# Kernel optimization log

Hardware: AMD Instinct MI355X
Metric: run time of the kernel (lower is better)

Reference implementation:

```python
import jax, jax.numpy as jnp
import numpy as np

N = 65536
E = 1048576
IN_DIM, HID, OUT = 500, 256, 64
ALPHA = 0.1
K = 10


def setup_inputs() -> dict:
    key = jax.random.key(0)
    ks = jax.random.split(key, 12)
    x = jax.random.normal(ks[0], (N, IN_DIM), dtype=jnp.float32)
    edge_row = jax.random.randint(ks[1], (E,), 0, N, dtype=jnp.int32)
    edge_col = jax.random.randint(ks[2], (E,), 0, N, dtype=jnp.int32)
    edge_weight = jax.random.uniform(ks[3], (E,), dtype=jnp.float32)
    # Linear params (Kaiming-uniform-like scale)
    def lin(k, fan_in, fan_out):
        kw, kb = jax.random.split(k)
        bound = 1.0 / np.sqrt(fan_in)
        W = jax.random.uniform(kw, (fan_in, fan_out), minval=-bound, maxval=bound, dtype=jnp.float32)
        b = jax.random.uniform(kb, (fan_out,), minval=-bound, maxval=bound, dtype=jnp.float32)
        return W, b
    W1, b1 = lin(ks[4], IN_DIM, HID)
    W2, b2 = lin(ks[5], HID, HID)
    W3, b3 = lin(ks[6], HID, OUT)
    return {"x": x, "W1": W1, "b1": b1, "W2": W2, "b2": b2,
            "W3": W3, "b3": b3, "edge_weight": edge_weight,
            "edge_row": edge_row, "edge_col": edge_col}


def reference(x, W1, b1, W2, b2, W3, b3, edge_weight, edge_row, edge_col):
    # MLP stack (dropout=0.0, norm_type='none')
    h = jax.nn.relu(x @ W1 + b1)          # [N, HID]
    h = jax.nn.relu(h @ W2 + b2)          # [N, HID]
    h = h @ W3 + b3                        # [N, OUT]
    h0 = h
    w = edge_weight[:, None]               # [E, 1]
    # APPNP: k steps of h = (1-alpha) * (A @ h) + alpha * h0 (SpMM via segment_sum)
    def step(h, _):
        msg = h[edge_col] * w               # [E, OUT] gather + scale
        agg = jax.ops.segment_sum(msg, edge_row, num_segments=N)  # [N, OUT]
        return (1.0 - ALPHA) * agg + ALPHA * h0, None
    h, _ = jax.lax.scan(step, h, None, length=K)
    return h
```

## Files before the change

### kernel.cpp

```cpp
#include <hip/hip_runtime.h>
#include <cstdint>
#include <cstddef>


#define N_NODES   65536
#define N_EDGES   1048576
#define IN_DIM    500
#define IN_PAD    512
#define HID_DIM   256
#define OUT_DIM   64
#define K_STEPS   10

#define NPW   8
#define CAPW  608
#define NCHUNK 16

typedef _Float16 half8 __attribute__((ext_vector_type(8)));
typedef float    f32x4 __attribute__((ext_vector_type(4)));

#define XB_OFF    0ULL
#define HA_OFF    0ULL
#define HB_OFF    33554432ULL
#define H1_OFF    67108864ULL
#define H0_OFF    67108864ULL
#define H2_OFF    100663296ULL
#define CNT2_OFF  100663296ULL
#define RANK_OFF  104857600ULL
#define TOT_OFF   109051904ULL
#define W1T_OFF   134217728ULL
#define W2T_OFF   134479872ULL
#define W3T_OFF   134610944ULL
#define ROWP_OFF  134643712ULL
#define EDG_OFF   135430400ULL

__device__ __forceinline__ void gload_lds16(const void* g, void* l) {
  __builtin_amdgcn_global_load_lds(
      (const __attribute__((address_space(1))) void*)g,
      (__attribute__((address_space(3))) void*)l, 16, 0, 0);
}

__device__ __forceinline__ unsigned short f2bf_rne(float f) {
  unsigned u = __float_as_uint(f);
  u += 0x7fffu + ((u >> 16) & 1u);
  return (unsigned short)(u >> 16);
}
__device__ __forceinline__ float uaf(int u) {
  return __uint_as_float((unsigned)u);
}
__device__ __forceinline__ float lo16(unsigned v) {
  return __uint_as_float(v << 16);
}
__device__ __forceinline__ float hi16(unsigned v) {
  return __uint_as_float(v & 0xffff0000u);
}

template <int TM, int TN, int WM, int WN, bool RELU, int OMODE>
__global__ __launch_bounds__(256)
void gemm_kernel(const _Float16* __restrict__ A, const _Float16* __restrict__ B,
                 const float* __restrict__ bias, void* __restrict__ Cout,
                 int M, int Nn, int K) {
  static_assert((TM * 8) % 256 == 0 && (TN * 8) % 256 == 0, "tile");
  __shared__ uint4 As[TM * 8];
  __shared__ uint4 Bs[TN * 8];
  const int t    = threadIdx.x;
  const int lane = t & 63;
  const int wave = t >> 6;
  const int wm   = wave / WN;
  const int wn   = wave % WN;
  const int row0 = blockIdx.x * TM;
  const int col0 = blockIdx.y * TN;
  const int l15  = lane & 15;
  const int lq   = lane >> 4;

  f32x4 acc[4][4];
#pragma unroll
  for (int i = 0; i < 4; ++i)
#pragma unroll
    for (int j = 0; j < 4; ++j) acc[i][j] = (f32x4){0.f, 0.f, 0.f, 0.f};

  for (int k0 = 0; k0 < K; k0 += 64) {
#pragma unroll
    for (int i = 0; i < (TM * 8) / 256; ++i) {
      const int c = i * 256 + wave * 64 + lane;
      const int q = c / TM;
      const int r = c % TM;
      gload_lds16(A + (size_t)(row0 + r) * K + (k0 + q * 8),
                  As + i * 256 + wave * 64);
    }
#pragma unroll
    for (int i = 0; i < (TN * 8) / 256; ++i) {
      const int c = i * 256 + wave * 64 + lane;
      const int q = c / TN;
      const int r = c % TN;
      gload_lds16(B + (size_t)(col0 + r) * K + (k0 + q * 8),
                  Bs + i * 256 + wave * 64);
    }
    __syncthreads();
#pragma unroll
    for (int kk = 0; kk < 2; ++kk) {
      const int qa = kk * 4 + lq;
      half8 af[4], bfr[4];
#pragma unroll
      for (int mt = 0; mt < 4; ++mt)
        af[mt] = *((const half8*)(As + (qa * TM + wm * 64 + mt * 16 + l15)));
#pragma unroll
      for (int nt = 0; nt < 4; ++nt)
        bfr[nt] = *((const half8*)(Bs + (qa * TN + wn * 64 + nt * 16 + l15)));
#pragma unroll
      for (int mt = 0; mt < 4; ++mt)
#pragma unroll
        for (int nt = 0; nt < 4; ++nt)
          acc[mt][nt] = __builtin_amdgcn_mfma_f32_16x16x32_f16(
              af[mt], bfr[nt], acc[mt][nt], 0, 0, 0);
    }
    __syncthreads();
  }

#pragma unroll
  for (int mt = 0; mt < 4; ++mt) {
#pragma unroll
    for (int nt = 0; nt < 4; ++nt) {
      const int col = col0 + wn * 64 + nt * 16 + l15;
      const float bv = bias[col];
#pragma unroll
      for (int r = 0; r < 4; ++r) {
        const int row = row0 + wm * 64 + mt * 16 + lq * 4 + r;
        float v = acc[mt][nt][r] + bv;
        if (RELU) v = fmaxf(v, 0.f);
        if (OMODE == 0)
          ((_Float16*)Cout)[(size_t)row * Nn + col] = (_Float16)v;
        else if (OMODE == 1)
          ((unsigned short*)Cout)[(size_t)row * Nn + col] = f2bf_rne(v);
        else
          ((float*)Cout)[(size_t)row * Nn + col] = v;
      }
    }
  }
}

__global__ void cast_x_kernel(const float* __restrict__ x,
                              _Float16* __restrict__ xb) {
  const int c = blockIdx.x * blockDim.x + threadIdx.x;
  if (c >= N_NODES * (IN_PAD / 8)) return;
  const int row = c >> 6;
  const int c8  = (c & 63) << 3;
  half8 o;
  if (c8 + 8 <= IN_DIM) {
    const float4* p = (const float4*)(x + (size_t)row * IN_DIM + c8);
    const float4 a = p[0], b = p[1];
    o[0] = (_Float16)a.x; o[1] = (_Float16)a.y;
    o[2] = (_Float16)a.z; o[3] = (_Float16)a.w;
    o[4] = (_Float16)b.x; o[5] = (_Float16)b.y;
    o[6] = (_Float16)b.z; o[7] = (_Float16)b.w;
  } else {
#pragma unroll
    for (int j = 0; j < 8; ++j) {
      const float v = (c8 + j < IN_DIM) ? x[(size_t)row * IN_DIM + c8 + j] : 0.f;
      o[j] = (_Float16)v;
    }
  }
  *(half8*)(xb + (size_t)c * 8) = o;
}

__global__ void cast_w_kernel(const float* __restrict__ W,
                              _Float16* __restrict__ Wt, int K, int Kpad,
                              int Nn) {
  const int idx = blockIdx.x * blockDim.x + threadIdx.x;
  if (idx >= Nn * Kpad) return;
  const int n = idx / Kpad;
  const int k = idx % Kpad;
  const float v = (k < K) ? W[(size_t)k * Nn + n] : 0.f;
  Wt[idx] = (_Float16)v;
}

__global__ void hist2_kernel(const int* __restrict__ row,
                             int* __restrict__ cnt2, int* __restrict__ rank,
                             int E) {
  const int e = blockIdx.x * blockDim.x + threadIdx.x;
  if (e < E)
    rank[e] = atomicAdd(&cnt2[(e >> 16) * N_NODES + row[e]], 1);
}

__global__ void scan_tot_kernel(const int* __restrict__ cnt2,
                                int* __restrict__ tot) {
  const int r = blockIdx.x * blockDim.x + threadIdx.x;
  int s = 0;
#pragma unroll
  for (int c = 0; c < NCHUNK; ++c) s += cnt2[c * N_NODES + r];
  tot[r] = s;
}

__global__ void scan_kernel(const int4* __restrict__ counts4,
                            int* __restrict__ rowptr) {
  __shared__ int part[1024];
  const int t = threadIdx.x;
  const int base = t * 16;
  int4 c[16];
  int s = 0;
#pragma unroll
  for (int i = 0; i < 16; ++i) {
    c[i] = counts4[base + i];
    s += c[i].x + c[i].y + c[i].z + c[i].w;
  }
  part[t] = s;
  __syncthreads();
  for (int off = 1; off < 1024; off <<= 1) {
    const int v = (t >= off) ? part[t - off] : 0;
    __syncthreads();
    part[t] += v;
    __syncthreads();
  }
  int run = (t == 0) ? 0 : part[t - 1];
#pragma unroll
  for (int i = 0; i < 16; ++i) {
    int4 r;
    r.x = run; run += c[i].x;
    r.y = run; run += c[i].y;
    r.z = run; run += c[i].z;
    r.w = run; run += c[i].w;
    ((int4*)rowptr)[base + i] = r;
  }
  if (t == 1023) rowptr[N_NODES] = run;
}

__global__ void chunkbase_kernel(int* __restrict__ cnt2,
                                 const int* __restrict__ rowptr) {
  const int r = blockIdx.x * blockDim.x + threadIdx.x;
  int run = rowptr[r];
#pragma unroll
  for (int c = 0; c < NCHUNK; ++c) {
    const int t = cnt2[c * N_NODES + r];
    cnt2[c * N_NODES + r] = run;
    run += t;
  }
}

__global__ void scatter2_kernel(const int* __restrict__ row,
                                const int* __restrict__ col,
                                const float* __restrict__ w,
                                const int* __restrict__ rank,
                                const int* __restrict__ cbase,
                                int2* __restrict__ edges, int E) {
  const int e = blockIdx.x * blockDim.x + threadIdx.x;
  if (e < E) {
    const int pos = cbase[(e >> 16) * N_NODES + row[e]] + rank[e];
    edges[pos] = make_int2(col[e], __float_as_int(w[e]));
  }
}

template <bool OUT_F32>
__global__ __launch_bounds__(256)
void prop_step(const unsigned short* __restrict__ hin,
               const unsigned short* __restrict__ h0,
               void* __restrict__ hout, const int* __restrict__ rowptr,
               const int2* __restrict__ edges) {
  __shared__ int2 eb[4][CAPW];
  const int wave = threadIdx.x >> 6;
  const int lane = threadIdx.x & 63;
  const int half = lane >> 5;
  const int lp   = lane & 31;
  const int node0 = (blockIdx.x * 4 + wave) * NPW;
  const unsigned* __restrict__ hin32 = (const unsigned*)hin;
  const unsigned* __restrict__ h032  = (const unsigned*)h0;

  const int rp  = rowptr[node0 + min(lane, NPW)];
  const int beg = __shfl(rp, 0);
  const int nE  = __shfl(rp, NPW) - beg;
  const int rrel = rp - beg;
  int2* __restrict__ ebw = eb[wave];

  const bool fast = (nE <= CAPW);
  if (fast) {
    for (int i = lane; i < nE; i += 64) ebw[i] = edges[beg + i];
    __builtin_amdgcn_s_waitcnt(0);
  }

  for (int i = 0; i < NPW; ++i) {
    const int nb = __shfl(rrel, i);
    const int ne = __shfl(rrel, i + 1);
    float ax0 = 0.f, ay0 = 0.f, ax1 = 0.f, ay1 = 0.f;
    int j = nb;
    if (fast) {
      for (; j + 8 <= ne; j += 8) {
        const int2 e0 = ebw[j + 0 + half];
        const int2 e1 = ebw[j + 2 + half];
        const int2 e2 = ebw[j + 4 + half];
        const int2 e3 = ebw[j + 6 + half];
        const unsigned v0 = hin32[(e0.x << 5) | lp];
        const unsigned v1 = hin32[(e1.x << 5) | lp];
        const unsigned v2 = hin32[(e2.x << 5) | lp];
        const unsigned v3 = hin32[(e3.x << 5) | lp];
        const float w0 = uaf(e0.y), w1 = uaf(e1.y);
        const float w2 = uaf(e2.y), w3 = uaf(e3.y);
        ax0 = fmaf(w0, lo16(v0), ax0); ay0 = fmaf(w0, hi16(v0), ay0);
        ax1 = fmaf(w1, lo16(v1), ax1); ay1 = fmaf(w1, hi16(v1), ay1);
        ax0 = fmaf(w2, lo16(v2), ax0); ay0 = fmaf(w2, hi16(v2), ay0);
        ax1 = fmaf(w3, lo16(v3), ax1); ay1 = fmaf(w3, hi16(v3), ay1);
      }
      for (; j + 2 <= ne; j += 2) {
        const int2 e = ebw[j + half];
        const unsigned v = hin32[(e.x << 5) | lp];
        const float w = uaf(e.y);
        ax0 = fmaf(w, lo16(v), ax0); ay0 = fmaf(w, hi16(v), ay0);
      }
      if (j < ne) {
        const int2 e = ebw[j];
        const unsigned v = hin32[(e.x << 5) | lp];
        const float w = half ? 0.f : uaf(e.y);
        ax0 = fmaf(w, lo16(v), ax0); ay0 = fmaf(w, hi16(v), ay0);
      }
    } else {
      for (; j < ne; j += 2) {
        const int idx = j + half;
        const int2 e = edges[beg + (idx < ne ? idx : ne - 1)];
        const float w = (idx < ne) ? uaf(e.y) : 0.f;
        const unsigned v = hin32[(e.x << 5) | lp];
        ax0 = fmaf(w, lo16(v), ax0); ay0 = fmaf(w, hi16(v), ay0);
      }
    }
    float sx = ax0 + ax1;
    float sy = ay0 + ay1;
    sx += __shfl_xor(sx, 32);
    sy += __shfl_xor(sy, 32);
    const int o32 = ((node0 + i) << 5) | lp;
    const unsigned h0v = h032[o32];
    const float r0 = 0.9f * sx + 0.1f * lo16(h0v);
    const float r1 = 0.9f * sy + 0.1f * hi16(h0v);
    if (half == 0) {
      if (OUT_F32) {
        ((float2*)hout)[o32] = make_float2(r0, r1);
      } else {
        ((unsigned*)hout)[o32] =
            (unsigned)f2bf_rne(r0) | ((unsigned)f2bf_rne(r1) << 16);
      }
    }
  }
}

extern "C" void kernel_launch(void* const* d_in, const int* in_sizes, int n_in,
                              void* d_out, int out_size, void* d_ws,
                              size_t ws_size, hipStream_t stream) {
  const float* x  = (const float*)d_in[0];
  const float* W1 = (const float*)d_in[1];
  const float* b1 = (const float*)d_in[2];
  const float* W2 = (const float*)d_in[3];
  const float* b2 = (const float*)d_in[4];
  const float* W3 = (const float*)d_in[5];
  const float* b3 = (const float*)d_in[6];
  const float* ew = (const float*)d_in[7];
  const int* erow = (const int*)d_in[8];
  const int* ecol = (const int*)d_in[9];

  char* ws = (char*)d_ws;
  _Float16* xb  = (_Float16*)(ws + XB_OFF);
  _Float16* h1  = (_Float16*)(ws + H1_OFF);
  _Float16* h2  = (_Float16*)(ws + H2_OFF);
  _Float16* w1t = (_Float16*)(ws + W1T_OFF);
  _Float16* w2t = (_Float16*)(ws + W2T_OFF);
  _Float16* w3t = (_Float16*)(ws + W3T_OFF);
  unsigned short* h0b = (unsigned short*)(ws + H0_OFF);
  unsigned short* hAb = (unsigned short*)(ws + HA_OFF);
  unsigned short* hBb = (unsigned short*)(ws + HB_OFF);
  int* rowp     = (int*)(ws + ROWP_OFF);
  int* cnt2     = (int*)(ws + CNT2_OFF);
  int* rankb    = (int*)(ws + RANK_OFF);
  int* tot      = (int*)(ws + TOT_OFF);
  int2* edges   = (int2*)(ws + EDG_OFF);
  float* outp   = (float*)d_out;

  hipMemsetAsync(cnt2, 0, NCHUNK * N_NODES * sizeof(int), stream);
  hist2_kernel<<<N_EDGES / 256, 256, 0, stream>>>(erow, cnt2, rankb, N_EDGES);
  scan_tot_kernel<<<N_NODES / 256, 256, 0, stream>>>(cnt2, tot);
  scan_kernel<<<1, 1024, 0, stream>>>((const int4*)tot, rowp);
  chunkbase_kernel<<<N_NODES / 256, 256, 0, stream>>>(cnt2, rowp);
  scatter2_kernel<<<N_EDGES / 256, 256, 0, stream>>>(erow, ecol, ew, rankb,
                                                     cnt2, edges, N_EDGES);

  cast_x_kernel<<<(N_NODES * (IN_PAD / 8)) / 256, 256, 0, stream>>>(x, xb);
  cast_w_kernel<<<(HID_DIM * IN_PAD) / 256, 256, 0, stream>>>(W1, w1t, IN_DIM,
                                                              IN_PAD, HID_DIM);
  cast_w_kernel<<<(HID_DIM * HID_DIM) / 256, 256, 0, stream>>>(
      W2, w2t, HID_DIM, HID_DIM, HID_DIM);
  cast_w_kernel<<<(OUT_DIM * HID_DIM) / 256, 256, 0, stream>>>(
      W3, w3t, HID_DIM, HID_DIM, OUT_DIM);

  gemm_kernel<128, 128, 2, 2, true, 0>
      <<<dim3(N_NODES / 128, HID_DIM / 128), 256, 0, stream>>>(
          xb, w1t, b1, h1, N_NODES, HID_DIM, IN_PAD);
  gemm_kernel<128, 128, 2, 2, true, 0>
      <<<dim3(N_NODES / 128, HID_DIM / 128), 256, 0, stream>>>(
          h1, w2t, b2, h2, N_NODES, HID_DIM, HID_DIM);
  gemm_kernel<256, 64, 4, 1, false, 1>
      <<<dim3(N_NODES / 256, 1), 256, 0, stream>>>(h2, w3t, b3, h0b, N_NODES,
                                                   OUT_DIM, HID_DIM);

  for (int s = 0; s < K_STEPS - 1; ++s) {
    const unsigned short* hin = (s == 0) ? h0b : ((s - 1) & 1 ? hBb : hAb);
    unsigned short* hout = (s & 1) ? hBb : hAb;
    prop_step<false><<<N_NODES / (4 * NPW), 256, 0, stream>>>(hin, h0b, hout,
                                                              rowp, edges);
  }
  prop_step<true><<<N_NODES / (4 * NPW), 256, 0, stream>>>(
      (K_STEPS - 2) & 1 ? hBb : hAb, h0b, outp, rowp, edges);
}
```

Before: 641.8 us.

## Remap SpMM lanes to 8 edges x 8 features with 16-byte gathers

Changes the propagation kernel's lane mapping. Previously each lane loaded 4 bytes of a bf16 row and a wave covered 2 edges at a time. Now each lane loads a uint4 (8 bf16 features), so a wave covers 8 edges concurrently and issues fewer, wider gather instructions. The cost is more accumulator registers and a three-level shuffle reduction across edge slots per node. It also makes the short-row remainder handling coarser.

```diff
diff --git a/kernel.cpp b/kernel.cpp
--- a/kernel.cpp
+++ b/kernel.cpp
@@ -52,6 +52,17 @@
 }
 __device__ __forceinline__ float hi16(unsigned v) {
   return __uint_as_float(v & 0xffff0000u);
+}
+
+__device__ __forceinline__ void fma8(float wt, uint4 v, float* acc) {
+  acc[0] = fmaf(wt, lo16(v.x), acc[0]);
+  acc[1] = fmaf(wt, hi16(v.x), acc[1]);
+  acc[2] = fmaf(wt, lo16(v.y), acc[2]);
+  acc[3] = fmaf(wt, hi16(v.y), acc[3]);
+  acc[4] = fmaf(wt, lo16(v.z), acc[4]);
+  acc[5] = fmaf(wt, hi16(v.z), acc[5]);
+  acc[6] = fmaf(wt, lo16(v.w), acc[6]);
+  acc[7] = fmaf(wt, hi16(v.w), acc[7]);
 }
 
 template <int TM, int TN, int WM, int WN, bool RELU, int OMODE>
@@ -255,13 +266,13 @@
                void* __restrict__ hout, const int* __restrict__ rowptr,
                const int2* __restrict__ edges) {
   __shared__ int2 eb[4][CAPW];
-  const int wave = threadIdx.x >> 6;
-  const int lane = threadIdx.x & 63;
-  const int half = lane >> 5;
-  const int lp   = lane & 31;
+  const int wave  = threadIdx.x >> 6;
+  const int lane  = threadIdx.x & 63;
+  const int eslot = lane >> 3;
+  const int fq    = lane & 7;
   const int node0 = (blockIdx.x * 4 + wave) * NPW;
-  const unsigned* __restrict__ hin32 = (const unsigned*)hin;
-  const unsigned* __restrict__ h032  = (const unsigned*)h0;
+  const uint4* __restrict__ hin4 = (const uint4*)hin;
+  const uint4* __restrict__ h04  = (const uint4*)h0;
 
   const int rp  = rowptr[node0 + min(lane, NPW)];
   const int beg = __shfl(rp, 0);
@@ -278,60 +289,71 @@
   for (int i = 0; i < NPW; ++i) {
     const int nb = __shfl(rrel, i);
     const int ne = __shfl(rrel, i + 1);
-    float ax0 = 0.f, ay0 = 0.f, ax1 = 0.f, ay1 = 0.f;
+    float acc[8];
+#pragma unroll
+    for (int k = 0; k < 8; ++k) acc[k] = 0.f;
     int j = nb;
     if (fast) {
+      for (; j + 16 <= ne; j += 16) {
+        const int2 e0 = ebw[j + eslot];
+        const int2 e1 = ebw[j + 8 + eslot];
+        const uint4 v0 = hin4[(e0.x << 3) | fq];
+        const uint4 v1 = hin4[(e1.x << 3) | fq];
+        const float w0 = uaf(e0.y);
+        const float w1 = uaf(e1.y);
+        fma8(w0, v0, acc);
+        fma8(w1, v1, acc);
+      }
       for (; j + 8 <= ne; j += 8) {
-        const int2 e0 = ebw[j + 0 + half];
-        const int2 e1 = ebw[j + 2 + half];
-        const int2 e2 = ebw[j + 4 + half];
-        const int2 e3 = ebw[j + 6 + half];
-        const unsigned v0 = hin32[(e0.x << 5) | lp];
-        const unsigned v1 = hin32[(e1.x << 5) | lp];
-        const unsigned v2 = hin32[(e2.x << 5) | lp];
-        const unsigned v3 = hin32[(e3.x << 5) | lp];
-        const float w0 = uaf(e0.y), w1 = uaf(e1.y);
-        const float w2 = uaf(e2.y), w3 = uaf(e3.y);
-        ax0 = fmaf(w0, lo16(v0), ax0); ay0 = fmaf(w0, hi16(v0), ay0);
-        ax1 = fmaf(w1, lo16(v1), ax1); ay1 = fmaf(w1, hi16(v1), ay1);
-        ax0 = fmaf(w2, lo16(v2), ax0); ay0 = fmaf(w2, hi16(v2), ay0);
-        ax1 = fmaf(w3, lo16(v3), ax1); ay1 = fmaf(w3, hi16(v3), ay1);
-      }
-      for (; j + 2 <= ne; j += 2) {
-        const int2 e = ebw[j + half];
-        const unsigned v = hin32[(e.x << 5) | lp];
-        const float w = uaf(e.y);
-        ax0 = fmaf(w, lo16(v), ax0); ay0 = fmaf(w, hi16(v), ay0);
+        const int2 e = ebw[j + eslot];
+        const uint4 v = hin4[(e.x << 3) | fq];
+        fma8(uaf(e.y), v, acc);
       }
       if (j < ne) {
-        const int2 e = ebw[j];
-        const unsigned v = hin32[(e.x << 5) | lp];
-        const float w = half ? 0.f : uaf(e.y);
-        ax0 = fmaf(w, lo16(v), ax0); ay0 = fmaf(w, hi16(v), ay0);
+        const int idx = j + eslot;
+        const int2 e = ebw[idx < ne ? idx : ne - 1];
+        const float w = (idx < ne) ? uaf(e.y) : 0.f;
+        const uint4 v = hin4[(e.x << 3) | fq];
+        fma8(w, v, acc);
       }
     } else {
-      for (; j < ne; j += 2) {
-        const int idx = j + half;
+      for (; j < ne; j += 8) {
+        const int idx = j + eslot;
         const int2 e = edges[beg + (idx < ne ? idx : ne - 1)];
         const float w = (idx < ne) ? uaf(e.y) : 0.f;
-        const unsigned v = hin32[(e.x << 5) | lp];
-        ax0 = fmaf(w, lo16(v), ax0); ay0 = fmaf(w, hi16(v), ay0);
-      }
-    }
-    float sx = ax0 + ax1;
-    float sy = ay0 + ay1;
-    sx += __shfl_xor(sx, 32);
-    sy += __shfl_xor(sy, 32);
-    const int o32 = ((node0 + i) << 5) | lp;
-    const unsigned h0v = h032[o32];
-    const float r0 = 0.9f * sx + 0.1f * lo16(h0v);
-    const float r1 = 0.9f * sy + 0.1f * hi16(h0v);
-    if (half == 0) {
+        const uint4 v = hin4[(e.x << 3) | fq];
+        fma8(w, v, acc);
+      }
+    }
+#pragma unroll
+    for (int k = 0; k < 8; ++k) {
+      acc[k] += __shfl_xor(acc[k], 8);
+      acc[k] += __shfl_xor(acc[k], 16);
+      acc[k] += __shfl_xor(acc[k], 32);
+    }
+    const int node = node0 + i;
+    if (eslot == 0) {
+      const uint4 h0v = h04[(node << 3) | fq];
+      float r[8];
+      r[0] = 0.9f * acc[0] + 0.1f * lo16(h0v.x);
+      r[1] = 0.9f * acc[1] + 0.1f * hi16(h0v.x);
+      r[2] = 0.9f * acc[2] + 0.1f * lo16(h0v.y);
+      r[3] = 0.9f * acc[3] + 0.1f * hi16(h0v.y);
+      r[4] = 0.9f * acc[4] + 0.1f * lo16(h0v.z);
+      r[5] = 0.9f * acc[5] + 0.1f * hi16(h0v.z);
+      r[6] = 0.9f * acc[6] + 0.1f * lo16(h0v.w);
+      r[7] = 0.9f * acc[7] + 0.1f * hi16(h0v.w);
       if (OUT_F32) {
-        ((float2*)hout)[o32] = make_float2(r0, r1);
+        float4* o = (float4*)hout + (((size_t)node) << 4) + (fq << 1);
+        o[0] = make_float4(r[0], r[1], r[2], r[3]);
+        o[1] = make_float4(r[4], r[5], r[6], r[7]);
       } else {
-        ((unsigned*)hout)[o32] =
-            (unsigned)f2bf_rne(r0) | ((unsigned)f2bf_rne(r1) << 16);
+        uint4 p;
+        p.x = (unsigned)f2bf_rne(r[0]) | ((unsigned)f2bf_rne(r[1]) << 16);
+        p.y = (unsigned)f2bf_rne(r[2]) | ((unsigned)f2bf_rne(r[3]) << 16);
+        p.z = (unsigned)f2bf_rne(r[4]) | ((unsigned)f2bf_rne(r[5]) << 16);
+        p.w = (unsigned)f2bf_rne(r[6]) | ((unsigned)f2bf_rne(r[7]) << 16);
+        ((uint4*)hout)[(node << 3) | fq] = p;
       }
     }
   }
```

Result: slower. 686.2 us (+6.9%).

## Bucket CSR edges by source-column quarter to localize gathers across waves

Applied to the files above, without the earlier changes.

The CSR build now sub-sorts each row's edges into four buckets by source-node quarter (col>>14) instead of by edge-index chunk. The propagation kernel walks the four quarters in order for all 8 nodes of a wave, keeping per-node accumulators in registers. The intent is that concurrently running waves gather from the same quarter of h at the same time, improving L2/MALL hit rates for the random gathers. The price is more loop overhead, a shorter unroll (2 edges per half instead of 4), extra shuffles for segment bounds, and the counter buffer moving to its own workspace region.

```diff
diff --git a/kernel.cpp b/kernel.cpp
--- a/kernel.cpp
+++ b/kernel.cpp
@@ -13,7 +13,7 @@
 
 #define NPW   8
 #define CAPW  608
-#define NCHUNK 16
+#define NCHUNK 4
 
 typedef _Float16 half8 __attribute__((ext_vector_type(8)));
 typedef float    f32x4 __attribute__((ext_vector_type(4)));
@@ -24,7 +24,6 @@
 #define H1_OFF    67108864ULL
 #define H0_OFF    67108864ULL
 #define H2_OFF    100663296ULL
-#define CNT2_OFF  100663296ULL
 #define RANK_OFF  104857600ULL
 #define TOT_OFF   109051904ULL
 #define W1T_OFF   134217728ULL
@@ -32,6 +31,7 @@
 #define W3T_OFF   134610944ULL
 #define ROWP_OFF  134643712ULL
 #define EDG_OFF   135430400ULL
+#define CNT2_OFF  143819008ULL
 
 __device__ __forceinline__ void gload_lds16(const void* g, void* l) {
   __builtin_amdgcn_global_load_lds(
@@ -174,11 +174,12 @@
 }
 
 __global__ void hist2_kernel(const int* __restrict__ row,
+                             const int* __restrict__ col,
                              int* __restrict__ cnt2, int* __restrict__ rank,
                              int E) {
   const int e = blockIdx.x * blockDim.x + threadIdx.x;
   if (e < E)
-    rank[e] = atomicAdd(&cnt2[(e >> 16) * N_NODES + row[e]], 1);
+    rank[e] = atomicAdd(&cnt2[(col[e] >> 14) * N_NODES + row[e]], 1);
 }
 
 __global__ void scan_tot_kernel(const int* __restrict__ cnt2,
@@ -243,7 +244,7 @@
                                 int2* __restrict__ edges, int E) {
   const int e = blockIdx.x * blockDim.x + threadIdx.x;
   if (e < E) {
-    const int pos = cbase[(e >> 16) * N_NODES + row[e]] + rank[e];
+    const int pos = cbase[(col[e] >> 14) * N_NODES + row[e]] + rank[e];
     edges[pos] = make_int2(col[e], __float_as_int(w[e]));
   }
 }
@@ -253,6 +254,7 @@
 void prop_step(const unsigned short* __restrict__ hin,
                const unsigned short* __restrict__ h0,
                void* __restrict__ hout, const int* __restrict__ rowptr,
+               const int* __restrict__ qstart,
                const int2* __restrict__ edges) {
   __shared__ int2 eb[4][CAPW];
   const int wave = threadIdx.x >> 6;
@@ -263,10 +265,13 @@
   const unsigned* __restrict__ hin32 = (const unsigned*)hin;
   const unsigned* __restrict__ h032  = (const unsigned*)h0;
 
-  const int rp  = rowptr[node0 + min(lane, NPW)];
-  const int beg = __shfl(rp, 0);
-  const int nE  = __shfl(rp, NPW) - beg;
-  const int rrel = rp - beg;
+  int rq = 0;
+  if (lane < 32)
+    rq = qstart[(lane >> 3) * N_NODES + node0 + (lane & 7)];
+  else if (lane == 32)
+    rq = rowptr[node0 + NPW];
+  const int beg = __shfl(rq, 0);
+  const int nE  = __shfl(rq, 32) - beg;
   int2* __restrict__ ebw = eb[wave];
 
   const bool fast = (nE <= CAPW);
@@ -275,51 +280,57 @@
     __builtin_amdgcn_s_waitcnt(0);
   }
 
+  float ax[NPW], ay[NPW];
+#pragma unroll
+  for (int i = 0; i < NPW; ++i) { ax[i] = 0.f; ay[i] = 0.f; }
+
+  for (int q = 0; q < 4; ++q) {
+    for (int i = 0; i < NPW; ++i) {
+      const int sb = __shfl(rq, q * 8 + i) - beg;
+      const int se = (q < 3) ? (__shfl(rq, q * 8 + 8 + i) - beg)
+                   : ((i < NPW - 1) ? (__shfl(rq, i + 1) - beg) : nE);
+      float a0 = 0.f, a1 = 0.f, b0 = 0.f, b1 = 0.f;
+      int j = sb;
+      if (fast) {
+        for (; j + 4 <= se; j += 4) {
+          const int2 e0 = ebw[j + half];
+          const int2 e1 = ebw[j + 2 + half];
+          const unsigned v0 = hin32[(e0.x << 5) | lp];
+          const unsigned v1 = hin32[(e1.x << 5) | lp];
+          const float w0 = uaf(e0.y), w1 = uaf(e1.y);
+          a0 = fmaf(w0, lo16(v0), a0); a1 = fmaf(w0, hi16(v0), a1);
+          b0 = fmaf(w1, lo16(v1), b0); b1 = fmaf(w1, hi16(v1), b1);
+        }
+        for (; j + 2 <= se; j += 2) {
+          const int2 e = ebw[j + half];
+          const unsigned v = hin32[(e.x << 5) | lp];
+          const float w = uaf(e.y);
+          a0 = fmaf(w, lo16(v), a0); a1 = fmaf(w, hi16(v), a1);
+        }
+        if (j < se) {
+          const int2 e = ebw[j];
+          const unsigned v = hin32[(e.x << 5) | lp];
+          const float w = half ? 0.f : uaf(e.y);
+          a0 = fmaf(w, lo16(v), a0); a1 = fmaf(w, hi16(v), a1);
+        }
+      } else {
+        for (; j < se; j += 2) {
+          const int idx = j + half;
+          const int2 e = edges[beg + (idx < se ? idx : se - 1)];
+          const float w = (idx < se) ? uaf(e.y) : 0.f;
+          const unsigned v = hin32[(e.x << 5) | lp];
+          a0 = fmaf(w, lo16(v), a0); a1 = fmaf(w, hi16(v), a1);
+        }
+      }
+      ax[i] += a0 + b0;
+      ay[i] += a1 + b1;
+    }
+  }
+
+#pragma unroll
   for (int i = 0; i < NPW; ++i) {
-    const int nb = __shfl(rrel, i);
-    const int ne = __shfl(rrel, i + 1);
-    float ax0 = 0.f, ay0 = 0.f, ax1 = 0.f, ay1 = 0.f;
-    int j = nb;
-    if (fast) {
-      for (; j + 8 <= ne; j += 8) {
-        const int2 e0 = ebw[j + 0 + half];
-        const int2 e1 = ebw[j + 2 + half];
-        const int2 e2 = ebw[j + 4 + half];
-        const int2 e3 = ebw[j + 6 + half];
-        const unsigned v0 = hin32[(e0.x << 5) | lp];
-        const unsigned v1 = hin32[(e1.x << 5) | lp];
-        const unsigned v2 = hin32[(e2.x << 5) | lp];
-        const unsigned v3 = hin32[(e3.x << 5) | lp];
-        const float w0 = uaf(e0.y), w1 = uaf(e1.y);
-        const float w2 = uaf(e2.y), w3 = uaf(e3.y);
-        ax0 = fmaf(w0, lo16(v0), ax0); ay0 = fmaf(w0, hi16(v0), ay0);
-        ax1 = fmaf(w1, lo16(v1), ax1); ay1 = fmaf(w1, hi16(v1), ay1);
-        ax0 = fmaf(w2, lo16(v2), ax0); ay0 = fmaf(w2, hi16(v2), ay0);
-        ax1 = fmaf(w3, lo16(v3), ax1); ay1 = fmaf(w3, hi16(v3), ay1);
-      }
-      for (; j + 2 <= ne; j += 2) {
-        const int2 e = ebw[j + half];
-        const unsigned v = hin32[(e.x << 5) | lp];
-        const float w = uaf(e.y);
-        ax0 = fmaf(w, lo16(v), ax0); ay0 = fmaf(w, hi16(v), ay0);
-      }
-      if (j < ne) {
-        const int2 e = ebw[j];
-        const unsigned v = hin32[(e.x << 5) | lp];
-        const float w = half ? 0.f : uaf(e.y);
-        ax0 = fmaf(w, lo16(v), ax0); ay0 = fmaf(w, hi16(v), ay0);
-      }
-    } else {
-      for (; j < ne; j += 2) {
-        const int idx = j + half;
-        const int2 e = edges[beg + (idx < ne ? idx : ne - 1)];
-        const float w = (idx < ne) ? uaf(e.y) : 0.f;
-        const unsigned v = hin32[(e.x << 5) | lp];
-        ax0 = fmaf(w, lo16(v), ax0); ay0 = fmaf(w, hi16(v), ay0);
-      }
-    }
-    float sx = ax0 + ax1;
-    float sy = ay0 + ay1;
+    float sx = ax[i];
+    float sy = ay[i];
     sx += __shfl_xor(sx, 32);
     sy += __shfl_xor(sy, 32);
     const int o32 = ((node0 + i) << 5) | lp;
@@ -369,7 +380,8 @@
   float* outp   = (float*)d_out;
 
   hipMemsetAsync(cnt2, 0, NCHUNK * N_NODES * sizeof(int), stream);
-  hist2_kernel<<<N_EDGES / 256, 256, 0, stream>>>(erow, cnt2, rankb, N_EDGES);
+  hist2_kernel<<<N_EDGES / 256, 256, 0, stream>>>(erow, ecol, cnt2, rankb,
+                                                  N_EDGES);
   scan_tot_kernel<<<N_NODES / 256, 256, 0, stream>>>(cnt2, tot);
   scan_kernel<<<1, 1024, 0, stream>>>((const int4*)tot, rowp);
   chunkbase_kernel<<<N_NODES / 256, 256, 0, stream>>>(cnt2, rowp);
@@ -397,9 +409,9 @@
   for (int s = 0; s < K_STEPS - 1; ++s) {
     const unsigned short* hin = (s == 0) ? h0b : ((s - 1) & 1 ? hBb : hAb);
     unsigned short* hout = (s & 1) ? hBb : hAb;
-    prop_step<false><<<N_NODES / (4 * NPW), 256, 0, stream>>>(hin, h0b, hout,
-                                                              rowp, edges);
+    prop_step<false><<<N_NODES / (4 * NPW), 256, 0, stream>>>(
+        hin, h0b, hout, rowp, cnt2, edges);
   }
   prop_step<true><<<N_NODES / (4 * NPW), 256, 0, stream>>>(
-      (K_STEPS - 2) & 1 ? hBb : hAb, h0b, outp, rowp, edges);
-}
+      (K_STEPS - 2) & 1 ? hBb : hAb, h0b, outp, rowp, cnt2, edges);
+}
```

Result: slower. 854.7 us (+33.2%).
